# Optimization experiments

Hardware: AMD Instinct MI355X
Metric: run time of the kernel (lower is better)

Reference implementation:

```python
import jax, jax.numpy as jnp
import numpy as np

N_NODES = 40000
N_EDGES = 640000
IN_CH = 128
HID = 32
HEADS = 4
OUT_CH = 112
NEG_SLOPE = 0.2  # PyG GATConv default LeakyReLU slope


def _gat_conv(x, src, dst, W, a_src, a_dst, bias, heads, ch, concat):
    # x: [N, F_in], W: [F_in, heads*ch], a_src/a_dst: [heads, ch], bias: [heads*ch] or [ch]
    N = x.shape[0]
    h = (x @ W).reshape(N, heads, ch)                       # [N, H, C]
    al_src = jnp.sum(h * a_src, axis=-1)                    # [N, H]
    al_dst = jnp.sum(h * a_dst, axis=-1)                    # [N, H]
    e = jax.nn.leaky_relu(al_src[src] + al_dst[dst], NEG_SLOPE)  # [E, H]
    # numerically stable segment softmax over incoming edges of each dst node
    m = jax.ops.segment_max(e, dst, num_segments=N)
    m = jnp.where(jnp.isfinite(m), m, 0.0)
    ex = jnp.exp(e - m[dst])
    den = jax.ops.segment_sum(ex, dst, num_segments=N)
    alpha = ex / (den[dst] + 1e-16)                         # [E, H]
    out = jax.ops.segment_sum(h[src] * alpha[:, :, None], dst, num_segments=N)  # [N, H, C]
    out = out.reshape(N, heads * ch) if concat else out.mean(axis=1)
    return out + bias


def setup_inputs() -> dict:
    key = jax.random.key(0)
    ks = jax.random.split(key, 10)
    x = jax.random.normal(ks[0], (N_NODES, IN_CH), dtype=jnp.float32)
    edge_index = jax.random.randint(ks[1], (2, N_EDGES), 0, N_NODES, dtype=jnp.int64)
    s1 = 1.0 / np.sqrt(IN_CH)
    s2 = 1.0 / np.sqrt(HID * HEADS)
    s3 = 1.0 / np.sqrt(HID)
    return {
        "x": x,
        "edge_index": edge_index,
        "W1": jax.random.normal(ks[2], (IN_CH, HEADS * HID), dtype=jnp.float32) * s1,
        "a_src1": jax.random.normal(ks[3], (HEADS, HID), dtype=jnp.float32) * s3,
        "a_dst1": jax.random.normal(ks[4], (HEADS, HID), dtype=jnp.float32) * s3,
        "b1": jnp.zeros((HEADS * HID,), dtype=jnp.float32),
        "W2": jax.random.normal(ks[5], (HEADS * HID, HID), dtype=jnp.float32) * s2,
        "a_src2": jax.random.normal(ks[6], (1, HID), dtype=jnp.float32) * s3,
        "a_dst2": jax.random.normal(ks[7], (1, HID), dtype=jnp.float32) * s3,
        "b2": jnp.zeros((HID,), dtype=jnp.float32),
        "W_out": jax.random.normal(ks[8], (HID, OUT_CH), dtype=jnp.float32) * s3,
        "b_out": jnp.zeros((OUT_CH,), dtype=jnp.float32),
    }


def reference(x, edge_index, W1, a_src1, a_dst1, b1, W2, a_src2, a_dst2, b2, W_out, b_out):
    N = x.shape[0]
    # PyG GATConv adds self-loops by default
    loops = jnp.arange(N, dtype=edge_index.dtype)
    src = jnp.concatenate([edge_index[0], loops])
    dst = jnp.concatenate([edge_index[1], loops])
    h = _gat_conv(x, src, dst, W1, a_src1, a_dst1, b1, HEADS, HID, concat=True)
    h = jax.nn.elu(h)  # dropout is identity in eval mode
    h = _gat_conv(h, src, dst, W2, a_src2, a_dst2, b2, 1, HID, concat=True)
    h = jax.nn.elu(h)
    return h @ W_out + b_out
```

## Files before the change

### kernel.cpp

```cpp
#include <hip/hip_runtime.h>

#define N_NODES 40000
#define E_EDGES 640000
#define E_TOT   (E_EDGES + N_NODES)
#define SCAN_BLOCKS ((N_NODES + 255) / 256)
#define G1_BLOCKS 625
#define HIST_BLOCKS ((E_EDGES + 255) / 256)

typedef unsigned int uint;
typedef unsigned short ushort;
typedef __attribute__((ext_vector_type(8))) short short8v;
typedef __attribute__((ext_vector_type(4))) float f32x4;

__device__ __forceinline__ ushort f2bf(float f) {
    uint u = __float_as_uint(f);
    u += 0x7FFFu + ((u >> 16) & 1u);
    return (ushort)(u >> 16);
}
__device__ __forceinline__ uint pk_bf(float lo, float hi) {
    return (uint)f2bf(lo) | ((uint)f2bf(hi) << 16);
}
__device__ __forceinline__ float bf_lo(uint w) { return __uint_as_float(w << 16); }
__device__ __forceinline__ float bf_hi(uint w) { return __uint_as_float(w & 0xFFFF0000u); }

__global__ __launch_bounds__(256) void prep_kernel(
    const float* __restrict__ W1, int4* __restrict__ cnt4, ushort* __restrict__ Wf)
{
    if (blockIdx.x < 40) {
        const int i = blockIdx.x * 256 + threadIdx.x;
        if (i < 40064 / 4) cnt4[i] = make_int4(1, 1, 1, 1);
        return;
    }
    const int s = (blockIdx.x - 40) * 256 + threadIdx.x;
    if (s >= 2048) return;
    const int kk = s >> 9;
    const int rem = s & 511;
    const int ct = rem >> 6;
    const int l = rem & 63;
    const int k0 = kk * 32 + (l >> 4) * 8;
    const int col = ct * 16 + (l & 15);
    uint4 o;
    o.x = pk_bf(W1[(k0 + 0) * 128 + col], W1[(k0 + 1) * 128 + col]);
    o.y = pk_bf(W1[(k0 + 2) * 128 + col], W1[(k0 + 3) * 128 + col]);
    o.z = pk_bf(W1[(k0 + 4) * 128 + col], W1[(k0 + 5) * 128 + col]);
    o.w = pk_bf(W1[(k0 + 6) * 128 + col], W1[(k0 + 7) * 128 + col]);
    ((uint4*)Wf)[s] = o;
}

__global__ __launch_bounds__(256) void gemm1_hist_kernel(
    const float* __restrict__ x, const ushort* __restrict__ Wf,
    const float* __restrict__ a_src, const float* __restrict__ a_dst,
    ushort* __restrict__ h1b, float* __restrict__ asrc, float* __restrict__ adst,
    const int* __restrict__ eidx, int* __restrict__ cnt, int* __restrict__ rank)
{
    if (blockIdx.x >= G1_BLOCKS) {
        const int e = (blockIdx.x - G1_BLOCKS) * 256 + threadIdx.x;
        if (e < E_EDGES)
            rank[e] = atomicAdd(&cnt[eidx[E_EDGES + e]], 1);
        return;
    }

    const int wv = threadIdx.x >> 6;
    const int lane = threadIdx.x & 63;
    const int rowbase = blockIdx.x * 64 + wv * 16;
    const int arow = rowbase + (lane & 15);
    const int kof = (lane >> 4) * 8;

    f32x4 acc0 = {0.f,0.f,0.f,0.f}, acc1 = {0.f,0.f,0.f,0.f};
    f32x4 acc2 = {0.f,0.f,0.f,0.f}, acc3 = {0.f,0.f,0.f,0.f};
    f32x4 acc4 = {0.f,0.f,0.f,0.f}, acc5 = {0.f,0.f,0.f,0.f};
    f32x4 acc6 = {0.f,0.f,0.f,0.f}, acc7 = {0.f,0.f,0.f,0.f};

    const short8v* WfV = (const short8v*)Wf;
#pragma unroll
    for (int kk = 0; kk < 4; ++kk) {
        const float* ap = &x[(size_t)arow * 128 + kk * 32 + kof];
        const float4 a0 = *(const float4*)ap;
        const float4 a1 = *(const float4*)(ap + 4);
        short8v af;
        af[0] = (short)f2bf(a0.x); af[1] = (short)f2bf(a0.y);
        af[2] = (short)f2bf(a0.z); af[3] = (short)f2bf(a0.w);
        af[4] = (short)f2bf(a1.x); af[5] = (short)f2bf(a1.y);
        af[6] = (short)f2bf(a1.z); af[7] = (short)f2bf(a1.w);
        const int base = kk * 8 * 64 + lane;
        acc0 = __builtin_amdgcn_mfma_f32_16x16x32_bf16(af, WfV[base + 0 * 64], acc0, 0, 0, 0);
        acc1 = __builtin_amdgcn_mfma_f32_16x16x32_bf16(af, WfV[base + 1 * 64], acc1, 0, 0, 0);
        acc2 = __builtin_amdgcn_mfma_f32_16x16x32_bf16(af, WfV[base + 2 * 64], acc2, 0, 0, 0);
        acc3 = __builtin_amdgcn_mfma_f32_16x16x32_bf16(af, WfV[base + 3 * 64], acc3, 0, 0, 0);
        acc4 = __builtin_amdgcn_mfma_f32_16x16x32_bf16(af, WfV[base + 4 * 64], acc4, 0, 0, 0);
        acc5 = __builtin_amdgcn_mfma_f32_16x16x32_bf16(af, WfV[base + 5 * 64], acc5, 0, 0, 0);
        acc6 = __builtin_amdgcn_mfma_f32_16x16x32_bf16(af, WfV[base + 6 * 64], acc6, 0, 0, 0);
        acc7 = __builtin_amdgcn_mfma_f32_16x16x32_bf16(af, WfV[base + 7 * 64], acc7, 0, 0, 0);
    }

    const int cl = lane & 15;
    const int rg = lane >> 4;
    float csA[8], cdA[8];
#pragma unroll
    for (int ct = 0; ct < 8; ++ct) {
        csA[ct] = a_src[(ct >> 1) * 32 + (ct & 1) * 16 + cl];
        cdA[ct] = a_dst[(ct >> 1) * 32 + (ct & 1) * 16 + cl];
    }
    const f32x4 accv[8] = { acc0, acc1, acc2, acc3, acc4, acc5, acc6, acc7 };
#pragma unroll
    for (int r = 0; r < 4; ++r) {
        const int n = rowbase + rg * 4 + r;
        ushort* hrow = &h1b[(size_t)n * 128 + cl];
#pragma unroll
        for (int ct = 0; ct < 8; ++ct) hrow[ct * 16] = f2bf(accv[ct][r]);
#pragma unroll
        for (int h = 0; h < 4; ++h) {
            float ps = accv[2 * h][r] * csA[2 * h] + accv[2 * h + 1][r] * csA[2 * h + 1];
            float pd = accv[2 * h][r] * cdA[2 * h] + accv[2 * h + 1][r] * cdA[2 * h + 1];
            ps += __shfl_xor(ps, 1); ps += __shfl_xor(ps, 2);
            ps += __shfl_xor(ps, 4); ps += __shfl_xor(ps, 8);
            pd += __shfl_xor(pd, 1); pd += __shfl_xor(pd, 2);
            pd += __shfl_xor(pd, 4); pd += __shfl_xor(pd, 8);
            if (cl == 0) { asrc[n * 4 + h] = ps; adst[n * 4 + h] = pd; }
        }
    }
}

__global__ __launch_bounds__(256) void scanA_kernel(
    const int* __restrict__ cnt, int* __restrict__ rowptr, int* __restrict__ bsum)
{
    const int i = blockIdx.x * 256 + threadIdx.x;
    const int lane = threadIdx.x & 63;
    const int wave = threadIdx.x >> 6;
    const int v = (i < N_NODES) ? cnt[i] : 0;
    int incl = v;
#pragma unroll
    for (int off = 1; off < 64; off <<= 1) {
        int u = __shfl_up(incl, off);
        if (lane >= off) incl += u;
    }
    __shared__ int ws[4];
    if (lane == 63) ws[wave] = incl;
    __syncthreads();
    int woff = 0;
    if (wave > 0) woff += ws[0];
    if (wave > 1) woff += ws[1];
    if (wave > 2) woff += ws[2];
    if (i <= N_NODES) rowptr[i] = woff + incl - v;
    if (threadIdx.x == 255) bsum[blockIdx.x] = woff + incl;
}

__global__ __launch_bounds__(256) void scanB_kernel(int* __restrict__ bsum)
{
    const int t = threadIdx.x;
    const int lane = t & 63;
    const int wave = t >> 6;
    const int v = (t < SCAN_BLOCKS) ? bsum[t] : 0;
    int incl = v;
#pragma unroll
    for (int off = 1; off < 64; off <<= 1) {
        int u = __shfl_up(incl, off);
        if (lane >= off) incl += u;
    }
    __shared__ int ws[4];
    if (lane == 63) ws[wave] = incl;
    __syncthreads();
    int woff = 0;
    if (wave > 0) woff += ws[0];
    if (wave > 1) woff += ws[1];
    if (wave > 2) woff += ws[2];
    if (t < SCAN_BLOCKS) bsum[t] = woff + incl - v;
}

__global__ __launch_bounds__(256) void fill_kernel(
    const int* __restrict__ eidx, const int* __restrict__ rowptr,
    const int* __restrict__ bsum, const int* __restrict__ rank,
    int* __restrict__ esrc)
{
    const int e = blockIdx.x * 256 + threadIdx.x;
    if (e >= E_TOT) return;
    int s, d, r;
    if (e < E_EDGES) { s = eidx[e]; d = eidx[E_EDGES + e]; r = rank[e]; }
    else             { s = d = e - E_EDGES; r = 0; }
    esrc[rowptr[d] + bsum[d >> 8] + r] = s;
}

__global__ __launch_bounds__(256) void gather1_kernel(
    const int* __restrict__ rowptr, const int* __restrict__ bsum,
    const int* __restrict__ esrc, const float* __restrict__ asrc,
    const float* __restrict__ adst,
    const ushort* __restrict__ h1b, const float* __restrict__ b,
    float* __restrict__ agg)
{
    const int t = blockIdx.x * 256 + threadIdx.x;
    const int node = t >> 5;
    const int l32 = t & 31;
    const int head = l32 >> 3;
    const int cb = l32 * 4;
    const float ad = adst[node * 4 + head];
    const int beg = rowptr[node] + bsum[node >> 8];
    const int end = rowptr[node + 1] + bsum[(node + 1) >> 8];
    float acc0 = 0.f, acc1 = 0.f, acc2 = 0.f, acc3 = 0.f, den = 0.f;

    int i = beg;
    for (; i + 8 <= end; i += 8) {
        int s[8];
        float a[8];
        uint2 w[8];
#pragma unroll
        for (int j = 0; j < 8; ++j) s[j] = esrc[i + j];
#pragma unroll
        for (int j = 0; j < 8; ++j) a[j] = asrc[s[j] * 4 + head];
#pragma unroll
        for (int j = 0; j < 8; ++j)
            w[j] = *(const uint2*)&h1b[(size_t)s[j] * 128 + cb];
#pragma unroll
        for (int j = 0; j < 8; ++j) {
            float v = a[j] + ad; v = v > 0.f ? v : 0.2f * v;
            const float e = __expf(v);
            den += e;
            acc0 = fmaf(e, bf_lo(w[j].x), acc0);
            acc1 = fmaf(e, bf_hi(w[j].x), acc1);
            acc2 = fmaf(e, bf_lo(w[j].y), acc2);
            acc3 = fmaf(e, bf_hi(w[j].y), acc3);
        }
    }
    for (; i < end; ++i) {
        const int s = esrc[i];
        float av = asrc[s * 4 + head] + ad;
        av = av > 0.f ? av : 0.2f * av;
        const float ex = __expf(av);
        const uint2 w = *(const uint2*)&h1b[(size_t)s * 128 + cb];
        den += ex;
        acc0 = fmaf(ex, bf_lo(w.x), acc0);
        acc1 = fmaf(ex, bf_hi(w.x), acc1);
        acc2 = fmaf(ex, bf_lo(w.y), acc2);
        acc3 = fmaf(ex, bf_hi(w.y), acc3);
    }

    const float inv = 1.f / (den + 1e-16f);
    const float4 bv = *(const float4*)&b[cb];
    float o0 = acc0 * inv + bv.x;
    float o1 = acc1 * inv + bv.y;
    float o2 = acc2 * inv + bv.z;
    float o3 = acc3 * inv + bv.w;
    o0 = o0 > 0.f ? o0 : expm1f(o0);
    o1 = o1 > 0.f ? o1 : expm1f(o1);
    o2 = o2 > 0.f ? o2 : expm1f(o2);
    o3 = o3 > 0.f ? o3 : expm1f(o3);
    *(float4*)&agg[(size_t)node * 128 + cb] = make_float4(o0, o1, o2, o3);
}

__global__ __launch_bounds__(256) void gemm2_kernel(
    const float* __restrict__ hin, const float* __restrict__ W,
    const float* __restrict__ a_src, const float* __restrict__ a_dst,
    float* __restrict__ h2, float* __restrict__ asrc, float* __restrict__ adst)
{
    __shared__ float Ws[128 * 32];
    {
        const float4* Wg = (const float4*)W;
        float4* Wl = (float4*)Ws;
        for (int i = threadIdx.x; i < 128 * 32 / 4; i += 256) Wl[i] = Wg[i];
    }
    __syncthreads();
    const int row0 = blockIdx.x * 64;
    const int tx = threadIdx.x & 7;
    const int ty = threadIdx.x >> 3;

    float acc[2][4];
#pragma unroll
    for (int r = 0; r < 2; ++r)
#pragma unroll
        for (int c = 0; c < 4; ++c) acc[r][c] = 0.f;

    for (int k0 = 0; k0 < 128; k0 += 4) {
        float xv[2][4];
#pragma unroll
        for (int r = 0; r < 2; ++r) {
            float4 t = *(const float4*)&hin[(size_t)(row0 + ty * 2 + r) * 128 + k0];
            xv[r][0] = t.x; xv[r][1] = t.y; xv[r][2] = t.z; xv[r][3] = t.w;
        }
#pragma unroll
        for (int kk = 0; kk < 4; ++kk) {
            float4 w = *(const float4*)&Ws[(k0 + kk) * 32 + tx * 4];
            float wreg[4] = { w.x, w.y, w.z, w.w };
#pragma unroll
            for (int r = 0; r < 2; ++r)
#pragma unroll
                for (int c = 0; c < 4; ++c)
                    acc[r][c] = fmaf(xv[r][kk], wreg[c], acc[r][c]);
        }
    }

    float as[4], ad[4];
#pragma unroll
    for (int c = 0; c < 4; ++c) {
        as[c] = a_src[tx * 4 + c];
        ad[c] = a_dst[tx * 4 + c];
    }
#pragma unroll
    for (int r = 0; r < 2; ++r) {
        const int n = row0 + ty * 2 + r;
        *(float4*)&h2[(size_t)n * 32 + tx * 4] =
            make_float4(acc[r][0], acc[r][1], acc[r][2], acc[r][3]);
        float ps = 0.f, pd = 0.f;
#pragma unroll
        for (int c = 0; c < 4; ++c) {
            ps = fmaf(acc[r][c], as[c], ps);
            pd = fmaf(acc[r][c], ad[c], pd);
        }
        ps += __shfl_xor(ps, 1); ps += __shfl_xor(ps, 2); ps += __shfl_xor(ps, 4);
        pd += __shfl_xor(pd, 1); pd += __shfl_xor(pd, 2); pd += __shfl_xor(pd, 4);
        if ((threadIdx.x & 7) == 0) { asrc[n] = ps; adst[n] = pd; }
    }
}

__global__ __launch_bounds__(256) void gather2_kernel(
    const int* __restrict__ rowptr, const int* __restrict__ bsum,
    const int* __restrict__ esrc,
    const float* __restrict__ asrc, const float* __restrict__ adst,
    const float* __restrict__ h2, const float* __restrict__ b,
    float* __restrict__ agg)
{
    const int t = blockIdx.x * 256 + threadIdx.x;
    const int node = t >> 5;
    const int c = t & 31;
    if (node >= N_NODES) return;
    const float ad = adst[node];
    const int beg = rowptr[node] + bsum[node >> 8];
    const int end = rowptr[node + 1] + bsum[(node + 1) >> 8];
    float acc = 0.f, den = 0.f;

    int i = beg;
    for (; i + 8 <= end; i += 8) {
        int s[8];
        float a[8], h[8];
#pragma unroll
        for (int j = 0; j < 8; ++j) s[j] = esrc[i + j];
#pragma unroll
        for (int j = 0; j < 8; ++j) a[j] = asrc[s[j]];
#pragma unroll
        for (int j = 0; j < 8; ++j) h[j] = h2[(size_t)s[j] * 32 + c];
#pragma unroll
        for (int j = 0; j < 8; ++j) {
            float v = a[j] + ad; v = v > 0.f ? v : 0.2f * v;
            const float e = __expf(v);
            den += e;
            acc = fmaf(e, h[j], acc);
        }
    }
    for (; i < end; ++i) {
        const int s = esrc[i];
        float av = asrc[s] + ad;
        av = av > 0.f ? av : 0.2f * av;
        const float ex = __expf(av);
        den += ex;
        acc = fmaf(ex, h2[(size_t)s * 32 + c], acc);
    }

    const float inv = 1.f / (den + 1e-16f);
    float o = acc * inv + b[c];
    o = o > 0.f ? o : expm1f(o);
    agg[(size_t)node * 32 + c] = o;
}

__global__ __launch_bounds__(256) void out_gemm_kernel(
    const float* __restrict__ h3, const float* __restrict__ W,
    const float* __restrict__ b, float* __restrict__ out)
{
    __shared__ float Ws[32 * 112];
    {
        const float4* Wg = (const float4*)W;
        float4* Wl = (float4*)Ws;
        for (int i = threadIdx.x; i < 32 * 112 / 4; i += 256) Wl[i] = Wg[i];
    }
    __syncthreads();
    const int row0 = blockIdx.x * 32;
    const int tc = threadIdx.x & 15;
    const int tr = threadIdx.x >> 4;

    float acc[2][7];
#pragma unroll
    for (int r = 0; r < 2; ++r)
#pragma unroll
        for (int c = 0; c < 7; ++c) acc[r][c] = 0.f;

    for (int k0 = 0; k0 < 32; k0 += 4) {
        float xv[2][4];
#pragma unroll
        for (int r = 0; r < 2; ++r) {
            float4 t = *(const float4*)&h3[(size_t)(row0 + tr * 2 + r) * 32 + k0];
            xv[r][0] = t.x; xv[r][1] = t.y; xv[r][2] = t.z; xv[r][3] = t.w;
        }
#pragma unroll
        for (int kk = 0; kk < 4; ++kk) {
            float wv[7];
#pragma unroll
            for (int c = 0; c < 7; ++c) wv[c] = Ws[(k0 + kk) * 112 + tc * 7 + c];
#pragma unroll
            for (int r = 0; r < 2; ++r)
#pragma unroll
                for (int c = 0; c < 7; ++c)
                    acc[r][c] = fmaf(xv[r][kk], wv[c], acc[r][c]);
        }
    }
#pragma unroll
    for (int r = 0; r < 2; ++r) {
        const int n = row0 + tr * 2 + r;
#pragma unroll
        for (int c = 0; c < 7; ++c)
            out[(size_t)n * 112 + tc * 7 + c] = acc[r][c] + b[tc * 7 + c];
    }
}

extern "C" void kernel_launch(void* const* d_in, const int* in_sizes, int n_in,
                              void* d_out, int out_size, void* d_ws, size_t ws_size,
                              hipStream_t stream) {
    const float* x      = (const float*)d_in[0];
    const int*   eidx   = (const int*)d_in[1];
    const float* W1     = (const float*)d_in[2];
    const float* a_src1 = (const float*)d_in[3];
    const float* a_dst1 = (const float*)d_in[4];
    const float* b1     = (const float*)d_in[5];
    const float* W2     = (const float*)d_in[6];
    const float* a_src2 = (const float*)d_in[7];
    const float* a_dst2 = (const float*)d_in[8];
    const float* b2     = (const float*)d_in[9];
    const float* W_out  = (const float*)d_in[10];
    const float* b_out  = (const float*)d_in[11];
    float* out = (float*)d_out;

    int* rowptr = (int*)d_ws;
    int* cnt    = rowptr + 40064;
    int* bsum   = cnt + 40064;
    int* rank   = bsum + 192;
    ushort* Wf  = (ushort*)(rank + 680000);
    int* esrc   = (int*)(Wf + 16384);
    ushort* h1b  = (ushort*)(esrc + 680000);
    float* asrc1 = (float*)(h1b + 5120000);
    float* adst1 = asrc1 + 160000;
    float* agg1  = adst1 + 160000;
    float* h2    = (float*)h1b;
    float* asrc2 = h2 + 1280000;
    float* adst2 = asrc2 + 40000;
    float* agg2  = adst2 + 40000;

    prep_kernel<<<48, 256, 0, stream>>>(W1, (int4*)cnt, Wf);

    gemm1_hist_kernel<<<G1_BLOCKS + HIST_BLOCKS, 256, 0, stream>>>(
        x, Wf, a_src1, a_dst1, h1b, asrc1, adst1, eidx, cnt, rank);

    scanA_kernel<<<SCAN_BLOCKS, 256, 0, stream>>>(cnt, rowptr, bsum);
    scanB_kernel<<<1, 256, 0, stream>>>(bsum);

    fill_kernel<<<(E_TOT + 255) / 256, 256, 0, stream>>>(
        eidx, rowptr, bsum, rank, esrc);

    gather1_kernel<<<5000, 256, 0, stream>>>(rowptr, bsum, esrc, asrc1, adst1,
                                             h1b, b1, agg1);

    gemm2_kernel<<<625, 256, 0, stream>>>(agg1, W2, a_src2, a_dst2, h2, asrc2, adst2);
    gather2_kernel<<<5000, 256, 0, stream>>>(rowptr, bsum, esrc, asrc2, adst2,
                                             h2, b2, agg2);

    out_gemm_kernel<<<1250, 256, 0, stream>>>(agg2, W_out, b_out, out);
}
```

Baseline: 133.0 us.

## Widen gather lanes, store layer-2 features in bf16, fuse two-pass scan

The two scan kernels become one, using a last-block-done atomic counter so the final block scans the block sums. Both gather kernels now use 16 threads per node instead of 32, so each thread loads wider vectors (16 bytes of bf16 in layer 1, bf16 pairs in layer 2). Layer-2 hidden features are stored as bf16 instead of fp32 to halve gather traffic. The aim is fewer launches, fewer memory transactions and less gather bandwidth, at the cost of reduced precision in layer 2 and fewer active threads per node.

```diff
diff --git a/kernel.cpp b/kernel.cpp
--- a/kernel.cpp
+++ b/kernel.cpp
@@ -24,8 +24,10 @@
 __device__ __forceinline__ float bf_hi(uint w) { return __uint_as_float(w & 0xFFFF0000u); }
 
 __global__ __launch_bounds__(256) void prep_kernel(
-    const float* __restrict__ W1, int4* __restrict__ cnt4, ushort* __restrict__ Wf)
-{
+    const float* __restrict__ W1, int4* __restrict__ cnt4, ushort* __restrict__ Wf,
+    int* __restrict__ done)
+{
+    if (blockIdx.x == 0 && threadIdx.x == 0) *done = 0;
     if (blockIdx.x < 40) {
         const int i = blockIdx.x * 256 + threadIdx.x;
         if (i < 40064 / 4) cnt4[i] = make_int4(1, 1, 1, 1);
@@ -121,8 +123,9 @@
     }
 }
 
-__global__ __launch_bounds__(256) void scanA_kernel(
-    const int* __restrict__ cnt, int* __restrict__ rowptr, int* __restrict__ bsum)
+__global__ __launch_bounds__(256) void scanAB_kernel(
+    const int* __restrict__ cnt, int* __restrict__ rowptr, int* __restrict__ bsum,
+    int* __restrict__ done)
 {
     const int i = blockIdx.x * 256 + threadIdx.x;
     const int lane = threadIdx.x & 63;
@@ -135,6 +138,7 @@
         if (lane >= off) incl += u;
     }
     __shared__ int ws[4];
+    __shared__ int isLast;
     if (lane == 63) ws[wave] = incl;
     __syncthreads();
     int woff = 0;
@@ -143,28 +147,29 @@
     if (wave > 2) woff += ws[2];
     if (i <= N_NODES) rowptr[i] = woff + incl - v;
     if (threadIdx.x == 255) bsum[blockIdx.x] = woff + incl;
-}
-
-__global__ __launch_bounds__(256) void scanB_kernel(int* __restrict__ bsum)
-{
+
+    __threadfence();
+    if (threadIdx.x == 0) isLast = (atomicAdd(done, 1) == SCAN_BLOCKS - 1);
+    __syncthreads();
+    if (!isLast) return;
+
     const int t = threadIdx.x;
-    const int lane = t & 63;
-    const int wave = t >> 6;
-    const int v = (t < SCAN_BLOCKS) ? bsum[t] : 0;
-    int incl = v;
+    int v2 = 0;
+    if (t < SCAN_BLOCKS) v2 = atomicAdd(&bsum[t], 0);
+    int incl2 = v2;
 #pragma unroll
     for (int off = 1; off < 64; off <<= 1) {
-        int u = __shfl_up(incl, off);
-        if (lane >= off) incl += u;
-    }
-    __shared__ int ws[4];
-    if (lane == 63) ws[wave] = incl;
-    __syncthreads();
-    int woff = 0;
-    if (wave > 0) woff += ws[0];
-    if (wave > 1) woff += ws[1];
-    if (wave > 2) woff += ws[2];
-    if (t < SCAN_BLOCKS) bsum[t] = woff + incl - v;
+        int u = __shfl_up(incl2, off);
+        if (lane >= off) incl2 += u;
+    }
+    __syncthreads();
+    if (lane == 63) ws[wave] = incl2;
+    __syncthreads();
+    int woff2 = 0;
+    if (wave > 0) woff2 += ws[0];
+    if (wave > 1) woff2 += ws[1];
+    if (wave > 2) woff2 += ws[2];
+    if (t < SCAN_BLOCKS) bsum[t] = woff2 + incl2 - v2;
 }
 
 __global__ __launch_bounds__(256) void fill_kernel(
@@ -188,27 +193,28 @@
     float* __restrict__ agg)
 {
     const int t = blockIdx.x * 256 + threadIdx.x;
-    const int node = t >> 5;
-    const int l32 = t & 31;
-    const int head = l32 >> 3;
-    const int cb = l32 * 4;
+    const int node = t >> 4;
+    const int l16 = t & 15;
+    const int head = l16 >> 2;
+    const int cb = l16 * 8;
     const float ad = adst[node * 4 + head];
     const int beg = rowptr[node] + bsum[node >> 8];
     const int end = rowptr[node + 1] + bsum[(node + 1) >> 8];
-    float acc0 = 0.f, acc1 = 0.f, acc2 = 0.f, acc3 = 0.f, den = 0.f;
+    float acc0 = 0.f, acc1 = 0.f, acc2 = 0.f, acc3 = 0.f;
+    float acc4 = 0.f, acc5 = 0.f, acc6 = 0.f, acc7 = 0.f, den = 0.f;
 
     int i = beg;
     for (; i + 8 <= end; i += 8) {
         int s[8];
         float a[8];
-        uint2 w[8];
+        uint4 w[8];
 #pragma unroll
         for (int j = 0; j < 8; ++j) s[j] = esrc[i + j];
 #pragma unroll
         for (int j = 0; j < 8; ++j) a[j] = asrc[s[j] * 4 + head];
 #pragma unroll
         for (int j = 0; j < 8; ++j)
-            w[j] = *(const uint2*)&h1b[(size_t)s[j] * 128 + cb];
+            w[j] = *(const uint4*)&h1b[(size_t)s[j] * 128 + cb];
 #pragma unroll
         for (int j = 0; j < 8; ++j) {
             float v = a[j] + ad; v = v > 0.f ? v : 0.2f * v;
@@ -218,6 +224,10 @@
             acc1 = fmaf(e, bf_hi(w[j].x), acc1);
             acc2 = fmaf(e, bf_lo(w[j].y), acc2);
             acc3 = fmaf(e, bf_hi(w[j].y), acc3);
+            acc4 = fmaf(e, bf_lo(w[j].z), acc4);
+            acc5 = fmaf(e, bf_hi(w[j].z), acc5);
+            acc6 = fmaf(e, bf_lo(w[j].w), acc6);
+            acc7 = fmaf(e, bf_hi(w[j].w), acc7);
         }
     }
     for (; i < end; ++i) {
@@ -225,31 +235,41 @@
         float av = asrc[s * 4 + head] + ad;
         av = av > 0.f ? av : 0.2f * av;
         const float ex = __expf(av);
-        const uint2 w = *(const uint2*)&h1b[(size_t)s * 128 + cb];
+        const uint4 w = *(const uint4*)&h1b[(size_t)s * 128 + cb];
         den += ex;
         acc0 = fmaf(ex, bf_lo(w.x), acc0);
         acc1 = fmaf(ex, bf_hi(w.x), acc1);
         acc2 = fmaf(ex, bf_lo(w.y), acc2);
         acc3 = fmaf(ex, bf_hi(w.y), acc3);
+        acc4 = fmaf(ex, bf_lo(w.z), acc4);
+        acc5 = fmaf(ex, bf_hi(w.z), acc5);
+        acc6 = fmaf(ex, bf_lo(w.w), acc6);
+        acc7 = fmaf(ex, bf_hi(w.w), acc7);
     }
 
     const float inv = 1.f / (den + 1e-16f);
-    const float4 bv = *(const float4*)&b[cb];
-    float o0 = acc0 * inv + bv.x;
-    float o1 = acc1 * inv + bv.y;
-    float o2 = acc2 * inv + bv.z;
-    float o3 = acc3 * inv + bv.w;
+    const float4 b0 = *(const float4*)&b[cb];
+    const float4 b1 = *(const float4*)&b[cb + 4];
+    float o0 = acc0 * inv + b0.x, o1 = acc1 * inv + b0.y;
+    float o2 = acc2 * inv + b0.z, o3 = acc3 * inv + b0.w;
+    float o4 = acc4 * inv + b1.x, o5 = acc5 * inv + b1.y;
+    float o6 = acc6 * inv + b1.z, o7 = acc7 * inv + b1.w;
     o0 = o0 > 0.f ? o0 : expm1f(o0);
     o1 = o1 > 0.f ? o1 : expm1f(o1);
     o2 = o2 > 0.f ? o2 : expm1f(o2);
     o3 = o3 > 0.f ? o3 : expm1f(o3);
-    *(float4*)&agg[(size_t)node * 128 + cb] = make_float4(o0, o1, o2, o3);
+    o4 = o4 > 0.f ? o4 : expm1f(o4);
+    o5 = o5 > 0.f ? o5 : expm1f(o5);
+    o6 = o6 > 0.f ? o6 : expm1f(o6);
+    o7 = o7 > 0.f ? o7 : expm1f(o7);
+    *(float4*)&agg[(size_t)node * 128 + cb]     = make_float4(o0, o1, o2, o3);
+    *(float4*)&agg[(size_t)node * 128 + cb + 4] = make_float4(o4, o5, o6, o7);
 }
 
 __global__ __launch_bounds__(256) void gemm2_kernel(
     const float* __restrict__ hin, const float* __restrict__ W,
     const float* __restrict__ a_src, const float* __restrict__ a_dst,
-    float* __restrict__ h2, float* __restrict__ asrc, float* __restrict__ adst)
+    ushort* __restrict__ h2b, float* __restrict__ asrc, float* __restrict__ adst)
 {
     __shared__ float Ws[128 * 32];
     {
@@ -296,8 +316,10 @@
 #pragma unroll
     for (int r = 0; r < 2; ++r) {
         const int n = row0 + ty * 2 + r;
-        *(float4*)&h2[(size_t)n * 32 + tx * 4] =
-            make_float4(acc[r][0], acc[r][1], acc[r][2], acc[r][3]);
+        uint2 o;
+        o.x = pk_bf(acc[r][0], acc[r][1]);
+        o.y = pk_bf(acc[r][2], acc[r][3]);
+        *(uint2*)&h2b[(size_t)n * 32 + tx * 4] = o;
         float ps = 0.f, pd = 0.f;
 #pragma unroll
         for (int c = 0; c < 4; ++c) {
@@ -314,34 +336,36 @@
     const int* __restrict__ rowptr, const int* __restrict__ bsum,
     const int* __restrict__ esrc,
     const float* __restrict__ asrc, const float* __restrict__ adst,
-    const float* __restrict__ h2, const float* __restrict__ b,
+    const ushort* __restrict__ h2b, const float* __restrict__ b,
     float* __restrict__ agg)
 {
     const int t = blockIdx.x * 256 + threadIdx.x;
-    const int node = t >> 5;
-    const int c = t & 31;
-    if (node >= N_NODES) return;
+    const int node = t >> 4;
+    const int c2 = (t & 15) * 2;
     const float ad = adst[node];
     const int beg = rowptr[node] + bsum[node >> 8];
     const int end = rowptr[node + 1] + bsum[(node + 1) >> 8];
-    float acc = 0.f, den = 0.f;
+    float acc0 = 0.f, acc1 = 0.f, den = 0.f;
 
     int i = beg;
     for (; i + 8 <= end; i += 8) {
         int s[8];
-        float a[8], h[8];
+        float a[8];
+        uint w[8];
 #pragma unroll
         for (int j = 0; j < 8; ++j) s[j] = esrc[i + j];
 #pragma unroll
         for (int j = 0; j < 8; ++j) a[j] = asrc[s[j]];
 #pragma unroll
-        for (int j = 0; j < 8; ++j) h[j] = h2[(size_t)s[j] * 32 + c];
+        for (int j = 0; j < 8; ++j)
+            w[j] = *(const uint*)&h2b[(size_t)s[j] * 32 + c2];
 #pragma unroll
         for (int j = 0; j < 8; ++j) {
             float v = a[j] + ad; v = v > 0.f ? v : 0.2f * v;
             const float e = __expf(v);
             den += e;
-            acc = fmaf(e, h[j], acc);
+            acc0 = fmaf(e, bf_lo(w[j]), acc0);
+            acc1 = fmaf(e, bf_hi(w[j]), acc1);
         }
     }
     for (; i < end; ++i) {
@@ -349,14 +373,19 @@
         float av = asrc[s] + ad;
         av = av > 0.f ? av : 0.2f * av;
         const float ex = __expf(av);
+        const uint w = *(const uint*)&h2b[(size_t)s * 32 + c2];
         den += ex;
-        acc = fmaf(ex, h2[(size_t)s * 32 + c], acc);
+        acc0 = fmaf(ex, bf_lo(w), acc0);
+        acc1 = fmaf(ex, bf_hi(w), acc1);
     }
 
     const float inv = 1.f / (den + 1e-16f);
-    float o = acc * inv + b[c];
-    o = o > 0.f ? o : expm1f(o);
-    agg[(size_t)node * 32 + c] = o;
+    const float2 bv = *(const float2*)&b[c2];
+    float o0 = acc0 * inv + bv.x;
+    float o1 = acc1 * inv + bv.y;
+    o0 = o0 > 0.f ? o0 : expm1f(o0);
+    o1 = o1 > 0.f ? o1 : expm1f(o1);
+    *(float2*)&agg[(size_t)node * 32 + c2] = make_float2(o0, o1);
 }
 
 __global__ __launch_bounds__(256) void out_gemm_kernel(
@@ -428,35 +457,35 @@
     int* rowptr = (int*)d_ws;
     int* cnt    = rowptr + 40064;
     int* bsum   = cnt + 40064;
-    int* rank   = bsum + 192;
+    int* done   = bsum + 192;
+    int* rank   = done + 16;
     ushort* Wf  = (ushort*)(rank + 680000);
     int* esrc   = (int*)(Wf + 16384);
     ushort* h1b  = (ushort*)(esrc + 680000);
     float* asrc1 = (float*)(h1b + 5120000);
     float* adst1 = asrc1 + 160000;
     float* agg1  = adst1 + 160000;
-    float* h2    = (float*)h1b;
-    float* asrc2 = h2 + 1280000;
+    ushort* h2b  = (ushort*)h1b;
+    float* asrc2 = (float*)(h2b + 1280000);
     float* adst2 = asrc2 + 40000;
     float* agg2  = adst2 + 40000;
 
-    prep_kernel<<<48, 256, 0, stream>>>(W1, (int4*)cnt, Wf);
+    prep_kernel<<<48, 256, 0, stream>>>(W1, (int4*)cnt, Wf, done);
 
     gemm1_hist_kernel<<<G1_BLOCKS + HIST_BLOCKS, 256, 0, stream>>>(
         x, Wf, a_src1, a_dst1, h1b, asrc1, adst1, eidx, cnt, rank);
 
-    scanA_kernel<<<SCAN_BLOCKS, 256, 0, stream>>>(cnt, rowptr, bsum);
-    scanB_kernel<<<1, 256, 0, stream>>>(bsum);
+    scanAB_kernel<<<SCAN_BLOCKS, 256, 0, stream>>>(cnt, rowptr, bsum, done);
 
     fill_kernel<<<(E_TOT + 255) / 256, 256, 0, stream>>>(
         eidx, rowptr, bsum, rank, esrc);
 
-    gather1_kernel<<<5000, 256, 0, stream>>>(rowptr, bsum, esrc, asrc1, adst1,
+    gather1_kernel<<<2500, 256, 0, stream>>>(rowptr, bsum, esrc, asrc1, adst1,
                                              h1b, b1, agg1);
 
-    gemm2_kernel<<<625, 256, 0, stream>>>(agg1, W2, a_src2, a_dst2, h2, asrc2, adst2);
-    gather2_kernel<<<5000, 256, 0, stream>>>(rowptr, bsum, esrc, asrc2, adst2,
-                                             h2, b2, agg2);
+    gemm2_kernel<<<625, 256, 0, stream>>>(agg1, W2, a_src2, a_dst2, h2b, asrc2, adst2);
+    gather2_kernel<<<2500, 256, 0, stream>>>(rowptr, bsum, esrc, asrc2, adst2,
+                                             h2b, b2, agg2);
 
     out_gemm_kernel<<<1250, 256, 0, stream>>>(agg2, W_out, b_out, out);
 }
```

Result: slower. 140.3 us (+5.5%).
